# Kernel optimization log

Hardware: AMD Instinct MI355X
Metric: run time of the kernel (lower is better)

The kernel has to match this reference:

```python
import jax, jax.numpy as jnp
import numpy as np

DIM = 256
HEADS = 8
HEAD_DIM = DIM // HEADS
FFN = 1024
DIST_DECAY = 10.0
SCALING = HEAD_DIM ** -0.5
EPS = 1e-5


def _layer_norm(x, g, b):
    mu = jnp.mean(x, axis=-1, keepdims=True)
    var = jnp.mean((x - mu) ** 2, axis=-1, keepdims=True)
    return (x - mu) * jax.lax.rsqrt(var + EPS) * g + b


def setup_inputs() -> dict:
    key = jax.random.key(0)
    ks = jax.random.split(key, 20)
    B, N = 2, 192
    p = lambda k, shape: (jax.random.normal(k, shape, dtype=jnp.float32) * 0.02)
    return {
        "x": jax.random.normal(ks[0], (B, N, DIM), dtype=jnp.float32),
        "pos": jax.random.normal(ks[1], (B, N, 3), dtype=jnp.float32),
        "mask": jax.random.randint(ks[2], (B, N), 0, 2).astype(bool),
        "Wqkv": p(ks[3], (DIM, 3 * DIM)), "bqkv": jnp.zeros((3 * DIM,), jnp.float32),
        "W1": p(ks[4], (1, 4 * DIM)), "b1": jnp.zeros((4 * DIM,), jnp.float32),
        "W2": p(ks[5], (4 * DIM, DIM)), "b2": jnp.zeros((DIM,), jnp.float32),
        "Wo": p(ks[6], (DIM, DIM)), "bo": jnp.zeros((DIM,), jnp.float32),
        "ln1_g": jnp.ones((DIM,), jnp.float32), "ln1_b": jnp.zeros((DIM,), jnp.float32),
        "Wf1": p(ks[7], (DIM, FFN)), "bf1": jnp.zeros((FFN,), jnp.float32),
        "Wf2": p(ks[8], (FFN, DIM)), "bf2": jnp.zeros((DIM,), jnp.float32),
        "ln2_g": jnp.ones((DIM,), jnp.float32), "ln2_b": jnp.zeros((DIM,), jnp.float32),
    }


def _attention(x, pos, mask, Wqkv, bqkv, W1, b1, W2, b2, Wo, bo):
    B, N, _ = x.shape
    qkv = x @ Wqkv + bqkv
    q, k, v = jnp.split(qkv, 3, axis=-1)  # each [B,N,dim]
    diff = pos[:, :, None, :] - pos[:, None, :, :]          # [B,N,N,3]
    sq = jnp.sum(diff * diff, axis=-1, keepdims=True)        # [B,N,N,1]
    # safe sqrt (dist is 0 on diagonal)
    dist = jnp.sqrt(jnp.where(sq > 0, sq, 1.0)) * (sq > 0)
    de = jax.nn.relu(dist @ W1 + b1) @ W2 + b2               # [B,N,N,dim]
    decay = jnp.exp(-sq / DIST_DECAY)                        # [B,N,N,1]
    # w[b,i,j] = decay_ij * (k_i + de_ij) * q_j * scale
    w = decay * ((k[:, :, None, :] + de) * q[:, None, :, :] * SCALING)
    w = w.reshape(B, N, N, HEADS, HEAD_DIM)
    pm = mask[:, :, None] & mask[:, None, :]                 # [B,N,N]
    w = jnp.where(pm[..., None, None], -jnp.inf, w)
    w = jax.nn.softmax(w, axis=2)                            # per-channel softmax over j
    out = jnp.sum(v.reshape(B, 1, N, HEADS, HEAD_DIM) * w, axis=2)
    out = out.reshape(B, N, DIM)
    return out @ Wo + bo


def reference(x, pos, mask, Wqkv, bqkv, W1, b1, W2, b2, Wo, bo,
              ln1_g, ln1_b, Wf1, bf1, Wf2, bf2, ln2_g, ln2_b):
    # post-norm (encoder_normalize_before=False), dropout=0 (eval)
    res = x
    a = _attention(x, pos, mask, Wqkv, bqkv, W1, b1, W2, b2, Wo, bo)
    x = _layer_norm(res + a, ln1_g, ln1_b)
    res = x
    h = jax.nn.relu(x @ Wf1 + bf1) @ Wf2 + bf2
    x = _layer_norm(res + h, ln2_g, ln2_b)
    return x
```

## Files before the change

### kernel.cpp

```cpp
#include <hip/hip_runtime.h>
#include <math.h>

#define NB 2
#define NN 192
#define DIMX 256
#define HID 1024
#define NROWS (NB * NN)
#define SCALING 0.17677669529663687f
#define EPS 1e-5f

#define OFF_KK    0
#define OFF_QVP   (OFF_KK + NROWS * DIMX)
#define OFF_TSORT (OFF_QVP + NROWS * DIMX)
#define OFF_IDX   (OFF_TSORT + HID)
#define OFF_SCP   (OFF_IDX + HID)
#define OFF_ATT   (OFF_SCP + (HID + 1) * DIMX)
#define OFF_WB    (OFF_ATT + NROWS * DIMX)
#define WB_WO  0
#define WB_WF1 32768
#define WB_WF2 163840
#define WB_TOT 294912

__device__ inline unsigned int f2b(float f) {
  const unsigned int u = __float_as_uint(f);
  return (u + 0x7fffu + ((u >> 16) & 1u)) >> 16;
}
__device__ inline float blo(unsigned int u) {
  return __uint_as_float(u << 16);
}
__device__ inline float bhi(unsigned int u) {
  return __uint_as_float(u & 0xffff0000u);
}

__global__ __launch_bounds__(1024) void prep_kernel(
    const float* __restrict__ x, const float* __restrict__ Wqkv,
    const float* __restrict__ bqkv, const float* __restrict__ W1,
    const float* __restrict__ b1, const float* __restrict__ Wo,
    const float* __restrict__ Wf1, const float* __restrict__ Wf2,
    float* __restrict__ kk, unsigned int* __restrict__ qvp,
    float* __restrict__ t_sorted, int* __restrict__ idx_sorted,
    unsigned int* __restrict__ wb) {
  __shared__ float xs[4][DIMX];
  __shared__ float red[4][4][768];
  __shared__ float ts[HID];
  __shared__ int part[64][17];
  const int tid = threadIdx.x;
  const int bx = blockIdx.x;
  if (bx < 96) {
    const int r0 = bx * 4;
    const int kc = tid >> 8;
    const int c = tid & 255;
    xs[tid >> 8][tid & 255] = x[(r0 + (tid >> 8)) * DIMX + (tid & 255)];
    __syncthreads();
    float acc[4][3];
#pragma unroll
    for (int rr = 0; rr < 4; ++rr)
      for (int u = 0; u < 3; ++u) acc[rr][u] = 0.f;
    const int k0 = kc * 64;
#pragma unroll 4
    for (int i = 0; i < 64; ++i) {
      const int k = k0 + i;
      const float w0 = Wqkv[k * 768 + c];
      const float w1 = Wqkv[k * 768 + 256 + c];
      const float w2 = Wqkv[k * 768 + 512 + c];
#pragma unroll
      for (int rr = 0; rr < 4; ++rr) {
        const float xv = xs[rr][k];
        acc[rr][0] += xv * w0;
        acc[rr][1] += xv * w1;
        acc[rr][2] += xv * w2;
      }
    }
#pragma unroll
    for (int rr = 0; rr < 4; ++rr) {
      red[kc][rr][c] = acc[rr][0];
      red[kc][rr][256 + c] = acc[rr][1];
      red[kc][rr][512 + c] = acc[rr][2];
    }
    __syncthreads();
    {
      const int rr = tid >> 8;
      const int row = r0 + rr;
      const float q = red[0][rr][c] + red[1][rr][c] + red[2][rr][c] +
                      red[3][rr][c] + bqkv[c];
      const float kkv = red[0][rr][256 + c] + red[1][rr][256 + c] +
                        red[2][rr][256 + c] + red[3][rr][256 + c] +
                        bqkv[256 + c];
      const float v = red[0][rr][512 + c] + red[1][rr][512 + c] +
                      red[2][rr][512 + c] + red[3][rr][512 + c] +
                      bqkv[512 + c];
      kk[row * DIMX + c] = kkv;
      qvp[row * DIMX + c] = f2b(q * SCALING) | (f2b(v) << 16);
    }
  } else if (bx < 112) {
    const int bk = bx - 96;
    {
      const float w = W1[tid];
      ts[tid] = (w != 0.f) ? (-b1[tid] / w) : INFINITY;
    }
    __syncthreads();
    const int hl = tid >> 4;
    const int ck = tid & 15;
    const int h = bk * 64 + hl;
    const float t = ts[h];
    int cnt = 0;
    const int r0 = ck * 64;
#pragma unroll 4
    for (int rr = 0; rr < 64; ++rr) {
      const int r = r0 + rr;
      const float tv = ts[r];
      cnt += ((tv < t) || (tv == t && r < h)) ? 1 : 0;
    }
    part[hl][ck] = cnt;
    __syncthreads();
    if (ck == 0) {
      int rank = 0;
#pragma unroll
      for (int u = 0; u < 16; ++u) rank += part[hl][u];
      t_sorted[rank] = t;
      idx_sorted[rank] = h;
    }
  } else {
    const int p = (bx - 112) * 1024 + tid;
    if (p < WB_TOT) {
      const float* src;
      int off;
      if (p < WB_WF1) { src = Wo; off = p; }
      else if (p < WB_WF2) { src = Wf1; off = p - WB_WF1; }
      else { src = Wf2; off = p - WB_WF2; }
      const float2 v = ((const float2*)src)[off];
      wb[p] = f2b(v.x) | (f2b(v.y) << 16);
    }
  }
}

__global__ __launch_bounds__(1024) void scan_kernel(
    const float* __restrict__ W1, const float* __restrict__ b1,
    const float* __restrict__ W2, const float* __restrict__ b2,
    const int* __restrict__ idx_sorted, unsigned int* __restrict__ SCp) {
  const int c = blockIdx.x;
  const int tid = threadIdx.x;
  const int lane = tid & 63;
  const int wid = tid >> 6;
  __shared__ float sW1[HID];
  __shared__ float sb1[HID];
  __shared__ int sidx[HID];
  __shared__ float bws[16], bwc[16], tws[16], twc[16];

  const float w = W1[tid];
  const float b1s = b1[tid];
  sW1[tid] = w;
  sb1[tid] = b1s;
  sidx[tid] = idx_sorted[tid];

  float bs = 0.f, bc = 0.f;
  {
    const float w2v = W2[tid * DIMX + c];
    if (w < 0.f) {
      bs = w * w2v;
      bc = b1s * w2v;
    } else if (w == 0.f && b1s > 0.f) {
      bc = b1s * w2v;
    }
  }
  for (int off = 32; off > 0; off >>= 1) {
    bs += __shfl_down(bs, off);
    bc += __shfl_down(bc, off);
  }
  __syncthreads();

  float vS, vC;
  {
    const int hh = sidx[tid];
    const float w1v = sW1[hh];
    const float sign = (w1v > 0.f) ? 1.f : -1.f;
    const float coefS = (w1v == 0.f) ? 0.f : sign * w1v;
    const float coefC = (w1v == 0.f) ? 0.f : sign * sb1[hh];
    const float w2v = W2[hh * DIMX + c];
    vS = coefS * w2v;
    vC = coefC * w2v;
  }
  for (int off = 1; off < 64; off <<= 1) {
    const float tS_ = __shfl_up(vS, off);
    const float tC_ = __shfl_up(vC, off);
    if (lane >= off) {
      vS += tS_;
      vC += tC_;
    }
  }
  if (lane == 0) {
    bws[wid] = bs;
    bwc[wid] = bc;
  }
  if (lane == 63) {
    tws[wid] = vS;
    twc[wid] = vC;
  }
  __syncthreads();
  float S0 = 0.f, C0 = 0.f, offS = 0.f, offC = 0.f;
#pragma unroll
  for (int u = 0; u < 16; ++u) {
    S0 += bws[u];
    C0 += bwc[u];
    if (u < wid) {
      offS += tws[u];
      offC += twc[u];
    }
  }
  C0 += b2[c];
  SCp[(tid + 1) * DIMX + c] = f2b(S0 + offS + vS) | (f2b(C0 + offC + vC) << 16);
  if (tid == 0) SCp[c] = f2b(S0) | (f2b(C0) << 16);
}

__global__ __launch_bounds__(1024) void attn_kernel(
    const float* __restrict__ pos, const int* __restrict__ mask,
    const float* __restrict__ kk, const unsigned int* __restrict__ qvp,
    const float* __restrict__ t_sorted, const unsigned int* __restrict__ SCp,
    float* __restrict__ att) {
  __shared__ float tS[HID];
  __shared__ float posB[NN][3];
  __shared__ int maskB[NN];
  __shared__ float dJ[NN];
  __shared__ float decJ[NN];
  __shared__ int segJ[NN];
  __shared__ int pmJ[NN];
  __shared__ float sl[4][DIMX];
  __shared__ float so[4][DIMX];

  const int r = blockIdx.x;
  const int b = r / NN;
  const int i = r % NN;
  const int tid = threadIdx.x;
  const int c = tid & 255;
  const int jq = tid >> 8;

  tS[tid] = t_sorted[tid];
  if (tid < NN) {
    posB[tid][0] = pos[(b * NN + tid) * 3 + 0];
    posB[tid][1] = pos[(b * NN + tid) * 3 + 1];
    posB[tid][2] = pos[(b * NN + tid) * 3 + 2];
    maskB[tid] = mask[b * NN + tid];
  }
  __syncthreads();

  if (tid < NN) {
    const int j = tid;
    const float dx = posB[j][0] - posB[i][0];
    const float dy = posB[j][1] - posB[i][1];
    const float dz = posB[j][2] - posB[i][2];
    const float sq = dx * dx + dy * dy + dz * dz;
    const float d = (sq > 0.f) ? sqrtf(sq) : 0.f;
    dJ[j] = d;
    decJ[j] = __expf(-sq * 0.1f);
    int lo = 0, hi = HID;
    while (lo < hi) {
      const int mid = (lo + hi) >> 1;
      if (tS[mid] <= d) lo = mid + 1;
      else hi = mid;
    }
    segJ[j] = lo;
    pmJ[j] = maskB[i] && maskB[j];
  }
  __syncthreads();

  const float kc_ = kk[(b * NN + i) * DIMX + c];
  float l = 0.f, o = 0.f;
  const int j0 = jq * 48;
#pragma unroll 4
  for (int jj = 0; jj < 48; ++jj) {
    const int j = j0 + jj;
    const int seg = segJ[j];
    const unsigned int scu = SCp[seg * DIMX + c];
    const float de = fmaf(dJ[j], blo(scu), bhi(scu));
    const unsigned int qvu = qvp[(b * NN + j) * DIMX + c];
    const float sval = decJ[j] * (kc_ + de) * blo(qvu);
    const float p = pmJ[j] ? 0.f : __expf(sval);
    l += p;
    o += p * bhi(qvu);
  }
  sl[jq][c] = l;
  so[jq][c] = o;
  __syncthreads();
  if (tid < DIMX) {
    const float lt = sl[0][tid] + sl[1][tid] + sl[2][tid] + sl[3][tid];
    const float ot = so[0][tid] + so[1][tid] + so[2][tid] + so[3][tid];
    att[r * DIMX + tid] = ot / lt;
  }
}

__global__ __launch_bounds__(1024) void tail_kernel(
    const float* __restrict__ att, const float* __restrict__ x,
    const uint2* __restrict__ WoB, const float* __restrict__ bo,
    const float* __restrict__ ln1g, const float* __restrict__ ln1b,
    const uint2* __restrict__ Wf1B, const float* __restrict__ bf1,
    const uint2* __restrict__ Wf2B, const float* __restrict__ bf2,
    const float* __restrict__ ln2g, const float* __restrict__ ln2b,
    float* __restrict__ out) {
  __shared__ float atts[2][DIMX];
  __shared__ float2 x1sT[DIMX];
  __shared__ float2 hidsT[HID];
  __shared__ float4 red[16][2][64];
  __shared__ float lr1[8], lr2[8];
  const int r0 = blockIdx.x * 2;
  const int tid = threadIdx.x;
  const int rr = tid >> 8;
  const int c = tid & 255;

  if (tid < 512) atts[rr][c] = att[(r0 + rr) * DIMX + c];
  __syncthreads();

  {
    const int ks = tid >> 6, c4 = tid & 63;
    float4 a0 = {0.f, 0.f, 0.f, 0.f}, a1 = {0.f, 0.f, 0.f, 0.f};
#pragma unroll
    for (int i = 0; i < 16; ++i) {
      const int k = ks * 16 + i;
      const uint2 wu = WoB[k * 64 + c4];
      const float w0 = blo(wu.x), w1 = bhi(wu.x), w2 = blo(wu.y), w3 = bhi(wu.y);
      const float v0 = atts[0][k], v1 = atts[1][k];
      a0.x += v0 * w0; a0.y += v0 * w1; a0.z += v0 * w2; a0.w += v0 * w3;
      a1.x += v1 * w0; a1.y += v1 * w1; a1.z += v1 * w2; a1.w += v1 * w3;
    }
    red[ks][0][c4] = a0;
    red[ks][1][c4] = a1;
  }
  __syncthreads();
  float t1 = 0.f, x1v = 0.f;
  if (rr < 2) {
    const float xr = x[(r0 + rr) * DIMX + c];
    const int c4 = c >> 2, cm = c & 3;
    float pv = 0.f;
#pragma unroll
    for (int u = 0; u < 16; ++u) pv += ((const float*)&red[u][rr][c4])[cm];
    t1 = pv + xr + bo[c];
  }
  {
    float s1 = t1, s2 = t1 * t1;
    for (int off = 32; off > 0; off >>= 1) {
      s1 += __shfl_down(s1, off);
      s2 += __shfl_down(s2, off);
    }
    if ((tid & 63) == 0 && tid < 512) { lr1[tid >> 6] = s1; lr2[tid >> 6] = s2; }
  }
  __syncthreads();
  if (rr < 2) {
    const int base = rr * 4;
    const float S1 = lr1[base] + lr1[base + 1] + lr1[base + 2] + lr1[base + 3];
    const float S2 = lr2[base] + lr2[base + 1] + lr2[base + 2] + lr2[base + 3];
    const float mu = S1 * (1.f / DIMX);
    const float var = S2 * (1.f / DIMX) - mu * mu;
    x1v = (t1 - mu) * rsqrtf(var + EPS) * ln1g[c] + ln1b[c];
    ((float*)&x1sT[c])[rr] = x1v;
  }
  __syncthreads();

  {
    const int ks = tid >> 8, h4 = tid & 255;
    float4 h0 = {0.f, 0.f, 0.f, 0.f}, h1 = {0.f, 0.f, 0.f, 0.f};
#pragma unroll 4
    for (int i = 0; i < 64; ++i) {
      const int k = ks * 64 + i;
      const uint2 wu = Wf1B[k * 256 + h4];
      const float w0 = blo(wu.x), w1 = bhi(wu.x), w2 = blo(wu.y), w3 = bhi(wu.y);
      const float2 xv = x1sT[k];
      h0.x += xv.x * w0; h0.y += xv.x * w1; h0.z += xv.x * w2; h0.w += xv.x * w3;
      h1.x += xv.y * w0; h1.y += xv.y * w1; h1.z += xv.y * w2; h1.w += xv.y * w3;
    }
    float4 (*redF)[2][256] = (float4(*)[2][256])red;
    redF[ks][0][h4] = h0;
    redF[ks][1][h4] = h1;
  }
  __syncthreads();
  {
    const int hh = tid;
    const int h4 = hh >> 2, cm = hh & 3;
    const float bf = bf1[hh];
    float4 (*redF)[2][256] = (float4(*)[2][256])red;
    const float v0 = ((const float*)&redF[0][0][h4])[cm] +
                     ((const float*)&redF[1][0][h4])[cm] +
                     ((const float*)&redF[2][0][h4])[cm] +
                     ((const float*)&redF[3][0][h4])[cm];
    const float v1 = ((const float*)&redF[0][1][h4])[cm] +
                     ((const float*)&redF[1][1][h4])[cm] +
                     ((const float*)&redF[2][1][h4])[cm] +
                     ((const float*)&redF[3][1][h4])[cm];
    __syncthreads();
    hidsT[hh] = make_float2(fmaxf(v0 + bf, 0.f), fmaxf(v1 + bf, 0.f));
  }
  __syncthreads();

  {
    const int ks = tid >> 6, c4 = tid & 63;
    float4 a0 = {0.f, 0.f, 0.f, 0.f}, a1 = {0.f, 0.f, 0.f, 0.f};
#pragma unroll 4
    for (int i = 0; i < 64; ++i) {
      const int k = ks * 64 + i;
      const uint2 wu = Wf2B[k * 64 + c4];
      const float w0 = blo(wu.x), w1 = bhi(wu.x), w2 = blo(wu.y), w3 = bhi(wu.y);
      const float2 hv = hidsT[k];
      a0.x += hv.x * w0; a0.y += hv.x * w1; a0.z += hv.x * w2; a0.w += hv.x * w3;
      a1.x += hv.y * w0; a1.y += hv.y * w1; a1.z += hv.y * w2; a1.w += hv.y * w3;
    }
    red[ks][0][c4] = a0;
    red[ks][1][c4] = a1;
  }
  __syncthreads();
  float t2 = 0.f;
  if (rr < 2) {
    const int c4 = c >> 2, cm = c & 3;
    float pv = 0.f;
#pragma unroll
    for (int u = 0; u < 16; ++u) pv += ((const float*)&red[u][rr][c4])[cm];
    t2 = pv + x1v + bf2[c];
  }
  {
    float s1 = t2, s2 = t2 * t2;
    for (int off = 32; off > 0; off >>= 1) {
      s1 += __shfl_down(s1, off);
      s2 += __shfl_down(s2, off);
    }
    if ((tid & 63) == 0 && tid < 512) { lr1[tid >> 6] = s1; lr2[tid >> 6] = s2; }
  }
  __syncthreads();
  if (rr < 2) {
    const int base = rr * 4;
    const float S1 = lr1[base] + lr1[base + 1] + lr1[base + 2] + lr1[base + 3];
    const float S2 = lr2[base] + lr2[base + 1] + lr2[base + 2] + lr2[base + 3];
    const float mu = S1 * (1.f / DIMX);
    const float var = S2 * (1.f / DIMX) - mu * mu;
    out[(r0 + rr) * DIMX + c] = (t2 - mu) * rsqrtf(var + EPS) * ln2g[c] + ln2b[c];
  }
}

extern "C" void kernel_launch(void* const* d_in, const int* in_sizes, int n_in,
                              void* d_out, int out_size, void* d_ws,
                              size_t ws_size, hipStream_t stream) {
  const float* x = (const float*)d_in[0];
  const float* pos = (const float*)d_in[1];
  const int* mask = (const int*)d_in[2];
  const float* Wqkv = (const float*)d_in[3];
  const float* bqkv = (const float*)d_in[4];
  const float* W1 = (const float*)d_in[5];
  const float* b1 = (const float*)d_in[6];
  const float* W2 = (const float*)d_in[7];
  const float* b2 = (const float*)d_in[8];
  const float* Wo = (const float*)d_in[9];
  const float* bo = (const float*)d_in[10];
  const float* ln1g = (const float*)d_in[11];
  const float* ln1b = (const float*)d_in[12];
  const float* Wf1 = (const float*)d_in[13];
  const float* bf1 = (const float*)d_in[14];
  const float* Wf2 = (const float*)d_in[15];
  const float* bf2 = (const float*)d_in[16];
  const float* ln2g = (const float*)d_in[17];
  const float* ln2b = (const float*)d_in[18];

  float* ws = (float*)d_ws;
  float* kk = ws + OFF_KK;
  unsigned int* qvp = (unsigned int*)(ws + OFF_QVP);
  float* t_sorted = ws + OFF_TSORT;
  int* idx_sorted = (int*)(ws + OFF_IDX);
  unsigned int* SCp = (unsigned int*)(ws + OFF_SCP);
  float* att = ws + OFF_ATT;
  unsigned int* wb = (unsigned int*)(ws + OFF_WB);
  float* outp = (float*)d_out;

  hipLaunchKernelGGL(prep_kernel, dim3(400), dim3(1024), 0, stream, x, Wqkv,
                     bqkv, W1, b1, Wo, Wf1, Wf2, kk, qvp, t_sorted, idx_sorted,
                     wb);
  hipLaunchKernelGGL(scan_kernel, dim3(DIMX), dim3(1024), 0, stream, W1, b1,
                     W2, b2, idx_sorted, SCp);
  hipLaunchKernelGGL(attn_kernel, dim3(NROWS), dim3(1024), 0, stream, pos,
                     mask, kk, qvp, t_sorted, SCp, att);
  hipLaunchKernelGGL(tail_kernel, dim3(NROWS / 2), dim3(1024), 0, stream, att,
                     x, (const uint2*)(wb + WB_WO), bo, ln1g, ln1b,
                     (const uint2*)(wb + WB_WF1), bf1,
                     (const uint2*)(wb + WB_WF2), bf2, ln2g, ln2b, outp);
}
```

Measured before the change: 61.24 us.

## Switch tail GEMVs to packed fp16 dot2 and use exp2 in attention

Weights for Wo, Wf1 and Wf2 are now packed into fp16 pairs along the reduction dimension, and the tail kernel's three matrix-vector products use v_dot2 (fdot2) on fp16-packed activations instead of unpacking bf16 and doing scalar FMAs. This halves the FMA count and changes the reduction and shared-memory layout. The attention loop folds log2(e) into the q scaling so it can use exp2f, and uses an explicit fma for the output accumulation. The tradeoff is fp16 range and precision for activations and weights, plus extra conversion passes through shared memory.

```diff
diff --git a/kernel.cpp b/kernel.cpp
--- a/kernel.cpp
+++ b/kernel.cpp
@@ -7,6 +7,7 @@
 #define HID 1024
 #define NROWS (NB * NN)
 #define SCALING 0.17677669529663687f
+#define LOG2E 1.4426950408889634f
 #define EPS 1e-5f
 
 #define OFF_KK    0
@@ -21,6 +22,8 @@
 #define WB_WF2 163840
 #define WB_TOT 294912
 
+typedef __fp16 half2_t __attribute__((ext_vector_type(2)));
+
 __device__ inline unsigned int f2b(float f) {
   const unsigned int u = __float_as_uint(f);
   return (u + 0x7fffu + ((u >> 16) & 1u)) >> 16;
@@ -30,6 +33,22 @@
 }
 __device__ inline float bhi(unsigned int u) {
   return __uint_as_float(u & 0xffff0000u);
+}
+__device__ inline unsigned int pkh(float a, float b) {
+  union { half2_t h; unsigned int u; } x;
+  x.h = __builtin_amdgcn_cvt_pkrtz(a, b);
+  return x.u;
+}
+__device__ inline unsigned int pkh_rn(float a, float b) {
+  union { half2_t h; unsigned int u; } x;
+  x.h = half2_t{(__fp16)a, (__fp16)b};
+  return x.u;
+}
+__device__ inline float fdot2u(unsigned int wu, unsigned int au, float c) {
+  union { unsigned int u; half2_t h; } w, a;
+  w.u = wu;
+  a.u = au;
+  return __builtin_amdgcn_fdot2(a.h, w.h, c, false);
 }
 
 __global__ __launch_bounds__(1024) void prep_kernel(
@@ -90,7 +109,7 @@
                       red[2][rr][512 + c] + red[3][rr][512 + c] +
                       bqkv[512 + c];
       kk[row * DIMX + c] = kkv;
-      qvp[row * DIMX + c] = f2b(q * SCALING) | (f2b(v) << 16);
+      qvp[row * DIMX + c] = f2b(q * (SCALING * LOG2E)) | (f2b(v) << 16);
     }
   } else if (bx < 112) {
     const int bk = bx - 96;
@@ -123,13 +142,23 @@
   } else {
     const int p = (bx - 112) * 1024 + tid;
     if (p < WB_TOT) {
-      const float* src;
-      int off;
-      if (p < WB_WF1) { src = Wo; off = p; }
-      else if (p < WB_WF2) { src = Wf1; off = p - WB_WF1; }
-      else { src = Wf2; off = p - WB_WF2; }
-      const float2 v = ((const float2*)src)[off];
-      wb[p] = f2b(v.x) | (f2b(v.y) << 16);
+      float a, b;
+      if (p < WB_WF1) {
+        const int kp = p >> 8, cc = p & 255;
+        a = Wo[(2 * kp) * DIMX + cc];
+        b = Wo[(2 * kp + 1) * DIMX + cc];
+      } else if (p < WB_WF2) {
+        const int q = p - WB_WF1;
+        const int kp = q >> 10, hh = q & 1023;
+        a = Wf1[(2 * kp) * HID + hh];
+        b = Wf1[(2 * kp + 1) * HID + hh];
+      } else {
+        const int q = p - WB_WF2;
+        const int kp = q >> 8, cc = q & 255;
+        a = Wf2[(2 * kp) * DIMX + cc];
+        b = Wf2[(2 * kp + 1) * DIMX + cc];
+      }
+      wb[p] = pkh_rn(a, b);
     }
   }
 }
@@ -273,10 +302,10 @@
     const unsigned int scu = SCp[seg * DIMX + c];
     const float de = fmaf(dJ[j], blo(scu), bhi(scu));
     const unsigned int qvu = qvp[(b * NN + j) * DIMX + c];
-    const float sval = decJ[j] * (kc_ + de) * blo(qvu);
-    const float p = pmJ[j] ? 0.f : __expf(sval);
+    const float sval = decJ[j] * blo(qvu) * (kc_ + de);
+    const float p = pmJ[j] ? 0.f : exp2f(sval);
     l += p;
-    o += p * bhi(qvu);
+    o = fmaf(p, bhi(qvu), o);
   }
   sl[jq][c] = l;
   so[jq][c] = o;
@@ -290,49 +319,52 @@
 
 __global__ __launch_bounds__(1024) void tail_kernel(
     const float* __restrict__ att, const float* __restrict__ x,
-    const uint2* __restrict__ WoB, const float* __restrict__ bo,
+    const unsigned int* __restrict__ woH, const float* __restrict__ bo,
     const float* __restrict__ ln1g, const float* __restrict__ ln1b,
-    const uint2* __restrict__ Wf1B, const float* __restrict__ bf1,
-    const uint2* __restrict__ Wf2B, const float* __restrict__ bf2,
+    const uint4* __restrict__ wf1H, const float* __restrict__ bf1,
+    const uint4* __restrict__ wf2H, const float* __restrict__ bf2,
     const float* __restrict__ ln2g, const float* __restrict__ ln2b,
     float* __restrict__ out) {
-  __shared__ float atts[2][DIMX];
-  __shared__ float2 x1sT[DIMX];
-  __shared__ float2 hidsT[HID];
   __shared__ float4 red[16][2][64];
+  __shared__ unsigned int attsH[2][128];
+  __shared__ unsigned int x1sH[2][128];
+  __shared__ unsigned int hidsH[2][512];
+  __shared__ float x1tmp[2][DIMX];
+  __shared__ float hidtmp[2][HID];
   __shared__ float lr1[8], lr2[8];
   const int r0 = blockIdx.x * 2;
   const int tid = threadIdx.x;
   const int rr = tid >> 8;
   const int c = tid & 255;
 
-  if (tid < 512) atts[rr][c] = att[(r0 + rr) * DIMX + c];
-  __syncthreads();
-
-  {
-    const int ks = tid >> 6, c4 = tid & 63;
-    float4 a0 = {0.f, 0.f, 0.f, 0.f}, a1 = {0.f, 0.f, 0.f, 0.f};
-#pragma unroll
-    for (int i = 0; i < 16; ++i) {
-      const int k = ks * 16 + i;
-      const uint2 wu = WoB[k * 64 + c4];
-      const float w0 = blo(wu.x), w1 = bhi(wu.x), w2 = blo(wu.y), w3 = bhi(wu.y);
-      const float v0 = atts[0][k], v1 = atts[1][k];
-      a0.x += v0 * w0; a0.y += v0 * w1; a0.z += v0 * w2; a0.w += v0 * w3;
-      a1.x += v1 * w0; a1.y += v1 * w1; a1.z += v1 * w2; a1.w += v1 * w3;
-    }
-    red[ks][0][c4] = a0;
-    red[ks][1][c4] = a1;
+  if (tid < 256) {
+    const int rr2 = tid >> 7, c2 = tid & 127;
+    const float2 f = ((const float2*)att)[(r0 + rr2) * 128 + c2];
+    attsH[rr2][c2] = pkh(f.x, f.y);
+  }
+  __syncthreads();
+
+  {
+    const int ks = tid >> 8;
+    float a0 = 0.f, a1 = 0.f;
+#pragma unroll 8
+    for (int i = 0; i < 32; ++i) {
+      const int kp = ks * 32 + i;
+      const unsigned int wu = woH[kp * 256 + c];
+      a0 = fdot2u(wu, attsH[0][kp], a0);
+      a1 = fdot2u(wu, attsH[1][kp], a1);
+    }
+    float* redp = (float*)red;
+    redp[(ks * 2 + 0) * 256 + c] = a0;
+    redp[(ks * 2 + 1) * 256 + c] = a1;
   }
   __syncthreads();
   float t1 = 0.f, x1v = 0.f;
   if (rr < 2) {
-    const float xr = x[(r0 + rr) * DIMX + c];
-    const int c4 = c >> 2, cm = c & 3;
-    float pv = 0.f;
-#pragma unroll
-    for (int u = 0; u < 16; ++u) pv += ((const float*)&red[u][rr][c4])[cm];
-    t1 = pv + xr + bo[c];
+    const float* redp = (const float*)red;
+    const float pv = redp[(0 * 2 + rr) * 256 + c] + redp[(1 * 2 + rr) * 256 + c] +
+                     redp[(2 * 2 + rr) * 256 + c] + redp[(3 * 2 + rr) * 256 + c];
+    t1 = pv + x[(r0 + rr) * DIMX + c] + bo[c];
   }
   {
     float s1 = t1, s2 = t1 * t1;
@@ -350,42 +382,51 @@
     const float mu = S1 * (1.f / DIMX);
     const float var = S2 * (1.f / DIMX) - mu * mu;
     x1v = (t1 - mu) * rsqrtf(var + EPS) * ln1g[c] + ln1b[c];
-    ((float*)&x1sT[c])[rr] = x1v;
+    x1tmp[rr][c] = x1v;
+  }
+  __syncthreads();
+  if (tid < 256) {
+    const int rr2 = tid >> 7, c2 = tid & 127;
+    x1sH[rr2][c2] = pkh(x1tmp[rr2][2 * c2], x1tmp[rr2][2 * c2 + 1]);
   }
   __syncthreads();
 
   {
     const int ks = tid >> 8, h4 = tid & 255;
-    float4 h0 = {0.f, 0.f, 0.f, 0.f}, h1 = {0.f, 0.f, 0.f, 0.f};
+    float4 a0 = {0.f, 0.f, 0.f, 0.f}, a1 = {0.f, 0.f, 0.f, 0.f};
 #pragma unroll 4
-    for (int i = 0; i < 64; ++i) {
-      const int k = ks * 64 + i;
-      const uint2 wu = Wf1B[k * 256 + h4];
-      const float w0 = blo(wu.x), w1 = bhi(wu.x), w2 = blo(wu.y), w3 = bhi(wu.y);
-      const float2 xv = x1sT[k];
-      h0.x += xv.x * w0; h0.y += xv.x * w1; h0.z += xv.x * w2; h0.w += xv.x * w3;
-      h1.x += xv.y * w0; h1.y += xv.y * w1; h1.z += xv.y * w2; h1.w += xv.y * w3;
-    }
-    float4 (*redF)[2][256] = (float4(*)[2][256])red;
-    redF[ks][0][h4] = h0;
-    redF[ks][1][h4] = h1;
-  }
-  __syncthreads();
-  {
-    const int hh = tid;
-    const int h4 = hh >> 2, cm = hh & 3;
-    const float bf = bf1[hh];
-    float4 (*redF)[2][256] = (float4(*)[2][256])red;
-    const float v0 = ((const float*)&redF[0][0][h4])[cm] +
-                     ((const float*)&redF[1][0][h4])[cm] +
-                     ((const float*)&redF[2][0][h4])[cm] +
-                     ((const float*)&redF[3][0][h4])[cm];
-    const float v1 = ((const float*)&redF[0][1][h4])[cm] +
-                     ((const float*)&redF[1][1][h4])[cm] +
-                     ((const float*)&redF[2][1][h4])[cm] +
-                     ((const float*)&redF[3][1][h4])[cm];
-    __syncthreads();
-    hidsT[hh] = make_float2(fmaxf(v0 + bf, 0.f), fmaxf(v1 + bf, 0.f));
+    for (int i = 0; i < 32; ++i) {
+      const int kp = ks * 32 + i;
+      const uint4 wv = wf1H[kp * 256 + h4];
+      const unsigned int xa = x1sH[0][kp], xb = x1sH[1][kp];
+      a0.x = fdot2u(wv.x, xa, a0.x);
+      a0.y = fdot2u(wv.y, xa, a0.y);
+      a0.z = fdot2u(wv.z, xa, a0.z);
+      a0.w = fdot2u(wv.w, xa, a0.w);
+      a1.x = fdot2u(wv.x, xb, a1.x);
+      a1.y = fdot2u(wv.y, xb, a1.y);
+      a1.z = fdot2u(wv.z, xb, a1.z);
+      a1.w = fdot2u(wv.w, xb, a1.w);
+    }
+    float4* redf4 = (float4*)red;
+    redf4[(ks * 2 + 0) * 256 + h4] = a0;
+    redf4[(ks * 2 + 1) * 256 + h4] = a1;
+  }
+  __syncthreads();
+  {
+    const float* redf = (const float*)red;
+    const float bf = bf1[tid];
+    const float v0 = redf[0 * 1024 + tid] + redf[2 * 1024 + tid] +
+                     redf[4 * 1024 + tid] + redf[6 * 1024 + tid];
+    const float v1 = redf[1 * 1024 + tid] + redf[3 * 1024 + tid] +
+                     redf[5 * 1024 + tid] + redf[7 * 1024 + tid];
+    hidtmp[0][tid] = fmaxf(v0 + bf, 0.f);
+    hidtmp[1][tid] = fmaxf(v1 + bf, 0.f);
+  }
+  __syncthreads();
+  {
+    const int rr2 = tid >> 9, c2 = tid & 511;
+    hidsH[rr2][c2] = pkh(hidtmp[rr2][2 * c2], hidtmp[rr2][2 * c2 + 1]);
   }
   __syncthreads();
 
@@ -393,13 +434,18 @@
     const int ks = tid >> 6, c4 = tid & 63;
     float4 a0 = {0.f, 0.f, 0.f, 0.f}, a1 = {0.f, 0.f, 0.f, 0.f};
 #pragma unroll 4
-    for (int i = 0; i < 64; ++i) {
-      const int k = ks * 64 + i;
-      const uint2 wu = Wf2B[k * 64 + c4];
-      const float w0 = blo(wu.x), w1 = bhi(wu.x), w2 = blo(wu.y), w3 = bhi(wu.y);
-      const float2 hv = hidsT[k];
-      a0.x += hv.x * w0; a0.y += hv.x * w1; a0.z += hv.x * w2; a0.w += hv.x * w3;
-      a1.x += hv.y * w0; a1.y += hv.y * w1; a1.z += hv.y * w2; a1.w += hv.y * w3;
+    for (int i = 0; i < 32; ++i) {
+      const int kp = ks * 32 + i;
+      const uint4 wv = wf2H[kp * 64 + c4];
+      const unsigned int ha = hidsH[0][kp], hb = hidsH[1][kp];
+      a0.x = fdot2u(wv.x, ha, a0.x);
+      a0.y = fdot2u(wv.y, ha, a0.y);
+      a0.z = fdot2u(wv.z, ha, a0.z);
+      a0.w = fdot2u(wv.w, ha, a0.w);
+      a1.x = fdot2u(wv.x, hb, a1.x);
+      a1.y = fdot2u(wv.y, hb, a1.y);
+      a1.z = fdot2u(wv.z, hb, a1.z);
+      a1.w = fdot2u(wv.w, hb, a1.w);
     }
     red[ks][0][c4] = a0;
     red[ks][1][c4] = a1;
@@ -473,7 +519,7 @@
   hipLaunchKernelGGL(attn_kernel, dim3(NROWS), dim3(1024), 0, stream, pos,
                      mask, kk, qvp, t_sorted, SCp, att);
   hipLaunchKernelGGL(tail_kernel, dim3(NROWS / 2), dim3(1024), 0, stream, att,
-                     x, (const uint2*)(wb + WB_WO), bo, ln1g, ln1b,
-                     (const uint2*)(wb + WB_WF1), bf1,
-                     (const uint2*)(wb + WB_WF2), bf2, ln2g, ln2b, outp);
-}
+                     x, (const unsigned int*)(wb + WB_WO), bo, ln1g, ln1b,
+                     (const uint4*)(wb + WB_WF1), bf1,
+                     (const uint4*)(wb + WB_WF2), bf2, ln2g, ln2b, outp);
+}
```

After: 57.98 us. 5.3% less time.
